# Kernel optimization log

Hardware: AMD Instinct MI355X
Metric: run time of the kernel (lower is better)

The kernel has to match this reference:

```python
import jax, jax.numpy as jnp
import numpy as np

NUM_F, K, EMB, N_NODE = 50000, 32, 128, 100000


def setup_inputs() -> dict:
    key = jax.random.key(0)
    k1, k2, k3, k4, k5, k6 = jax.random.split(key, 6)
    stdv = 1.0 / np.sqrt(EMB)
    return {
        "adjacency_fi": jax.random.randint(k1, (NUM_F, K), 0, N_NODE, dtype=jnp.int64)
        if jax.config.jax_enable_x64 else jax.random.randint(k1, (NUM_F, K), 0, N_NODE, dtype=jnp.int32),
        "embedding_i": jax.random.normal(k2, (N_NODE, EMB), dtype=jnp.float32),
        "embedding_f_weight": jax.random.uniform(k3, (NUM_F, EMB), jnp.float32, -stdv, stdv),
        "u": jax.random.uniform(k4, (EMB, 1), jnp.float32, -stdv, stdv),
        "W_weight": jax.random.uniform(k5, (EMB, 2 * EMB), jnp.float32, -stdv, stdv),
        "W_bias": jax.random.uniform(k6, (EMB,), jnp.float32, -stdv, stdv),
    }


def reference(adjacency_fi, embedding_i, embedding_f_weight, u, W_weight, W_bias):
    # Gather neighbor embeddings: [F, K, E]
    neigh = embedding_i[adjacency_fi]
    # Rank-1 attention score with additive padding mask (index 0 = pad)
    mask = jnp.where(adjacency_fi != 0, 0.0, -10000.0).astype(neigh.dtype)  # [F, K]
    alpha = jnp.einsum("fke,eo->fk", neigh, u) + mask
    alpha = jax.nn.softmax(alpha, axis=-1)
    agg = jnp.einsum("fk,fke->fe", alpha, neigh)  # [F, E]  (dropout70: eval mode, identity)
    # Gated fusion: gate = sigmoid(Linear(cat([emb_f, agg])))
    cat = jnp.concatenate([embedding_f_weight, agg], axis=1)  # [F, 2E]
    gate = jax.nn.sigmoid(cat @ W_weight.T + W_bias)  # [F, E]
    new_emb = gate * embedding_f_weight + (1.0 - gate) * agg  # (dropout50: eval mode, identity)
    return new_emb
```

## Files before the change

### kernel.cpp

```cpp
#include <hip/hip_runtime.h>

#define F_TOTAL 50000
#define N_NODE  100000
#define KNBR    32
#define EMB     128
#define FB      16
#define RPW     4

__global__ __launch_bounds__(256)
void node_scores(const float* __restrict__ embi,
                 const float* __restrict__ u,
                 float*       __restrict__ y)
{
    const int wave = threadIdx.x >> 6;
    const int lane = threadIdx.x & 63;
    const float2 uv = *(const float2*)(u + 2 * lane);

    const int base = (blockIdx.x * 4 + wave) * 8;

    float v[8];
#pragma unroll
    for (int j = 0; j < 8; ++j) {
        const float2 e = *(const float2*)(embi + (size_t)(base + j) * EMB + 2 * lane);
        v[j] = e.x * uv.x + e.y * uv.y;
    }

#pragma unroll
    for (int bit = 4; bit >= 1; bit >>= 1) {
        const bool upper = (lane & bit) != 0;
#pragma unroll
        for (int j = 0; j < bit; ++j) {
            const float send = upper ? v[j] : v[j + bit];
            const float recv = __shfl_xor(send, bit);
            v[j] = (upper ? v[j + bit] : v[j]) + recv;
        }
    }
    float d = v[0];
    d += __shfl_xor(d, 8);
    d += __shfl_xor(d, 16);
    d += __shfl_xor(d, 32);

    if (lane < 8) y[base + lane] = d;
}

__global__ __launch_bounds__(256, 4)
void fused_gnn(const int*   __restrict__ adj,
               const float* __restrict__ embi,
               const float* __restrict__ embf,
               const float* __restrict__ y,
               const float* __restrict__ W,
               const float* __restrict__ bias,
               float*       __restrict__ out)
{
    __shared__ float catbuf[FB][2 * EMB];
    __shared__ float pbuf[FB][EMB];

    const int tid   = threadIdx.x;
    const int wave  = tid >> 6;
    const int lane  = tid & 63;
    const int fbase = blockIdx.x * FB;

    for (int i = 0; i < RPW; ++i) {
        const int r = wave * RPW + i;
        const int f = fbase + r;

        const int myidx = adj[f * KNBR + (lane & 31)];

        float alpha = y[myidx] + ((myidx != 0) ? 0.0f : -10000.0f);

        float mx = alpha;
#pragma unroll
        for (int bit = 1; bit <= 16; bit <<= 1)
            mx = fmaxf(mx, __shfl_xor(mx, bit));
        const float e = __expf(alpha - mx);
        float s = e;
#pragma unroll
        for (int bit = 1; bit <= 16; bit <<= 1)
            s += __shfl_xor(s, bit);
        const float an = e / s;

        const float2 ef = *(const float2*)(embf + (size_t)f * EMB + 2 * lane);

        float2 nbA[8], nbB[8];
#pragma unroll
        for (int j = 0; j < 8; ++j) {
            const unsigned ik = (unsigned)__builtin_amdgcn_readlane(myidx, j);
            nbA[j] = *(const float2*)(embi + (size_t)ik * EMB + 2 * lane);
        }

        float2 acc = make_float2(0.f, 0.f);
#pragma unroll
        for (int g = 0; g < 4; ++g) {
            float2* cur = (g & 1) ? nbB : nbA;
            float2* nxt = (g & 1) ? nbA : nbB;
            if (g < 3) {
#pragma unroll
                for (int j = 0; j < 8; ++j) {
                    const unsigned ik =
                        (unsigned)__builtin_amdgcn_readlane(myidx, (g + 1) * 8 + j);
                    nxt[j] = *(const float2*)(embi + (size_t)ik * EMB + 2 * lane);
                }
            }
#pragma unroll
            for (int j = 0; j < 8; ++j) {
                const float a = __uint_as_float((unsigned)__builtin_amdgcn_readlane(
                    (int)__float_as_uint(an), g * 8 + j));
                acc.x = fmaf(a, cur[j].x, acc.x);
                acc.y = fmaf(a, cur[j].y, acc.y);
            }
        }

        *(float2*)&catbuf[r][2 * lane]       = ef;
        *(float2*)&catbuf[r][EMB + 2 * lane] = acc;
    }
    __syncthreads();

    const int p  = tid & 63;
    const int g  = tid >> 6;
    const int c0 = 2 * p, c1 = c0 + 1;
    const int jbase = g * 64;

    float acc0[FB], acc1[FB];
#pragma unroll
    for (int r = 0; r < FB; ++r) { acc0[r] = 0.f; acc1[r] = 0.f; }

    const float* W0 = W + (size_t)c0 * (2 * EMB) + jbase;
    const float* W1 = W + (size_t)c1 * (2 * EMB) + jbase;

#pragma unroll 4
    for (int j = 0; j < 64; j += 4) {
        const float4 w0 = *(const float4*)(W0 + j);
        const float4 w1 = *(const float4*)(W1 + j);
#pragma unroll
        for (int r = 0; r < FB; ++r) {
            const float4 cv = *(const float4*)&catbuf[r][jbase + j];
            acc0[r] += cv.x * w0.x + cv.y * w0.y + cv.z * w0.z + cv.w * w0.w;
            acc1[r] += cv.x * w1.x + cv.y * w1.y + cv.z * w1.z + cv.w * w1.w;
        }
    }

    if (g == 3) {
#pragma unroll
        for (int r = 0; r < FB; ++r) { pbuf[r][c0] = acc0[r]; pbuf[r][c1] = acc1[r]; }
    }
    __syncthreads();
    if (g == 2) {
#pragma unroll
        for (int r = 0; r < FB; ++r) { pbuf[r][c0] += acc0[r]; pbuf[r][c1] += acc1[r]; }
    }
    __syncthreads();
    if (g == 1) {
#pragma unroll
        for (int r = 0; r < FB; ++r) { pbuf[r][c0] += acc0[r]; pbuf[r][c1] += acc1[r]; }
    }
    __syncthreads();
    if (g == 0) {
        const float2 bv = *(const float2*)(bias + c0);
#pragma unroll
        for (int r = 0; r < FB; ++r) {
            const float t0 = acc0[r] + pbuf[r][c0] + bv.x;
            const float t1 = acc1[r] + pbuf[r][c1] + bv.y;
            const float g0 = 1.f / (1.f + __expf(-t0));
            const float g1 = 1.f / (1.f + __expf(-t1));
            const float e0 = catbuf[r][c0],       e1 = catbuf[r][c1];
            const float a0 = catbuf[r][EMB + c0], a1 = catbuf[r][EMB + c1];
            float2 o;
            o.x = g0 * e0 + (1.f - g0) * a0;
            o.y = g1 * e1 + (1.f - g1) * a1;
            *(float2*)(out + (size_t)(fbase + r) * EMB + c0) = o;
        }
    }
}

extern "C" void kernel_launch(void* const* d_in, const int* in_sizes, int n_in,
                              void* d_out, int out_size, void* d_ws, size_t ws_size,
                              hipStream_t stream) {
    const int*   adj  = (const int*)  d_in[0];
    const float* embi = (const float*)d_in[1];
    const float* embf = (const float*)d_in[2];
    const float* u    = (const float*)d_in[3];
    const float* W    = (const float*)d_in[4];
    const float* bias = (const float*)d_in[5];
    float* outp = (float*)d_out;
    float* y    = (float*)d_ws;

    node_scores<<<3125, 256, 0, stream>>>(embi, u, y);
    fused_gnn<<<F_TOTAL / FB, 256, 0, stream>>>(adj, embi, embf, y, W, bias, outp);
}
```

Before: 261.1 us.

## Split fused GNN kernel into separate attention-aggregation and gate-fusion kernels

Splits the single fused kernel into two. The first gathers neighbours and runs the softmax-weighted aggregation, writing the result to the output buffer with no LDS use. The second reads embf and that aggregate back into shared memory and runs the gated linear fusion in place. The goal is higher occupancy for the gather kernel, since it drops LDS and the min-blocks bound, and it also removes the double-buffered prefetch. The cost is an extra kernel launch and a full round trip of the aggregate through global memory.

```diff
diff --git a/kernel.cpp b/kernel.cpp
--- a/kernel.cpp
+++ b/kernel.cpp
@@ -43,21 +43,14 @@
     if (lane < 8) y[base + lane] = d;
 }
 
-__global__ __launch_bounds__(256, 4)
-void fused_gnn(const int*   __restrict__ adj,
-               const float* __restrict__ embi,
-               const float* __restrict__ embf,
-               const float* __restrict__ y,
-               const float* __restrict__ W,
-               const float* __restrict__ bias,
-               float*       __restrict__ out)
+__global__ __launch_bounds__(256)
+void attn_agg(const int*   __restrict__ adj,
+              const float* __restrict__ embi,
+              const float* __restrict__ y,
+              float*       __restrict__ agg)
 {
-    __shared__ float catbuf[FB][2 * EMB];
-    __shared__ float pbuf[FB][EMB];
-
-    const int tid   = threadIdx.x;
-    const int wave  = tid >> 6;
-    const int lane  = tid & 63;
+    const int wave  = threadIdx.x >> 6;
+    const int lane  = threadIdx.x & 63;
     const int fbase = blockIdx.x * FB;
 
     for (int i = 0; i < RPW; ++i) {
@@ -79,39 +72,50 @@
             s += __shfl_xor(s, bit);
         const float an = e / s;
 
-        const float2 ef = *(const float2*)(embf + (size_t)f * EMB + 2 * lane);
-
-        float2 nbA[8], nbB[8];
-#pragma unroll
-        for (int j = 0; j < 8; ++j) {
-            const unsigned ik = (unsigned)__builtin_amdgcn_readlane(myidx, j);
-            nbA[j] = *(const float2*)(embi + (size_t)ik * EMB + 2 * lane);
-        }
-
         float2 acc = make_float2(0.f, 0.f);
 #pragma unroll
-        for (int g = 0; g < 4; ++g) {
-            float2* cur = (g & 1) ? nbB : nbA;
-            float2* nxt = (g & 1) ? nbA : nbB;
-            if (g < 3) {
+        for (int c = 0; c < KNBR / 8; ++c) {
+            float2 nb[8];
 #pragma unroll
-                for (int j = 0; j < 8; ++j) {
-                    const unsigned ik =
-                        (unsigned)__builtin_amdgcn_readlane(myidx, (g + 1) * 8 + j);
-                    nxt[j] = *(const float2*)(embi + (size_t)ik * EMB + 2 * lane);
-                }
+            for (int j = 0; j < 8; ++j) {
+                const unsigned ik =
+                    (unsigned)__builtin_amdgcn_readlane(myidx, c * 8 + j);
+                nb[j] = *(const float2*)(embi + (size_t)ik * EMB + 2 * lane);
             }
 #pragma unroll
             for (int j = 0; j < 8; ++j) {
                 const float a = __uint_as_float((unsigned)__builtin_amdgcn_readlane(
-                    (int)__float_as_uint(an), g * 8 + j));
-                acc.x = fmaf(a, cur[j].x, acc.x);
-                acc.y = fmaf(a, cur[j].y, acc.y);
+                    (int)__float_as_uint(an), c * 8 + j));
+                acc.x = fmaf(a, nb[j].x, acc.x);
+                acc.y = fmaf(a, nb[j].y, acc.y);
             }
         }
 
-        *(float2*)&catbuf[r][2 * lane]       = ef;
-        *(float2*)&catbuf[r][EMB + 2 * lane] = acc;
+        *(float2*)(agg + (size_t)f * EMB + 2 * lane) = acc;
+    }
+}
+
+__global__ __launch_bounds__(256)
+void gate_fuse(const float* __restrict__ embf,
+               const float* __restrict__ W,
+               const float* __restrict__ bias,
+               float*       __restrict__ out)
+{
+    __shared__ float catbuf[FB][2 * EMB];
+    __shared__ float pbuf[FB][EMB];
+
+    const int tid   = threadIdx.x;
+    const int fbase = blockIdx.x * FB;
+
+#pragma unroll
+    for (int q = 0; q < 2; ++q) {
+        const int idx = q * 256 + tid;
+        const int r   = idx >> 5;
+        const int c   = (idx & 31) * 4;
+        *(float4*)&catbuf[r][c] =
+            *(const float4*)(embf + (size_t)(fbase + r) * EMB + c);
+        *(float4*)&catbuf[r][EMB + c] =
+            *(const float4*)(out + (size_t)(fbase + r) * EMB + c);
     }
     __syncthreads();
 
@@ -185,5 +189,6 @@
     float* y    = (float*)d_ws;
 
     node_scores<<<3125, 256, 0, stream>>>(embi, u, y);
-    fused_gnn<<<F_TOTAL / FB, 256, 0, stream>>>(adj, embi, embf, y, W, bias, outp);
+    attn_agg  <<<F_TOTAL / FB, 256, 0, stream>>>(adj, embi, y, outp);
+    gate_fuse <<<F_TOTAL / FB, 256, 0, stream>>>(embf, W, bias, outp);
 }
```

After: 292.5 us. +12.0%, slower.
